# Kernel optimization log

Measured on AMD Instinct MI355X. Metric: run time of the kernel, lower is better.

The kernel has to match this reference:

```python
import jax, jax.numpy as jnp
import numpy as np

NUM_GROUPS = 32
EPS = 1e-6


def group_norm(x, scale, bias):
    # x: [b, c, l]
    b, c, l = x.shape
    xg = x.reshape(b, NUM_GROUPS, (c // NUM_GROUPS) * l)
    mean = jnp.mean(xg, axis=2, keepdims=True)
    var = jnp.var(xg, axis=2, keepdims=True)
    xn = ((xg - mean) * jax.lax.rsqrt(var + EPS)).reshape(b, c, l)
    return xn * scale[None, :, None] + bias[None, :, None]


def conv1x1(x, w, b):
    # pointwise conv: w [out_c, in_c], x [b, in_c, l]
    return jnp.einsum('oc,bcl->bol', w, x) + b[None, :, None]


def setup_inputs() -> dict:
    key = jax.random.key(0)
    ks = jax.random.split(key, 11)
    b, c, l = 4, 512, 4096
    s = 1.0 / np.sqrt(c)
    return {
        'x': jax.random.normal(ks[0], (b, c, l), jnp.float32),
        'gn_scale': jnp.ones((c,), jnp.float32),
        'gn_bias': jnp.zeros((c,), jnp.float32),
        'wq': jax.random.normal(ks[1], (c, c), jnp.float32) * s,
        'bq': jnp.zeros((c,), jnp.float32),
        'wk': jax.random.normal(ks[2], (c, c), jnp.float32) * s,
        'bk': jnp.zeros((c,), jnp.float32),
        'wv': jax.random.normal(ks[3], (c, c), jnp.float32) * s,
        'bv': jnp.zeros((c,), jnp.float32),
        'wp': jax.random.normal(ks[4], (c, c), jnp.float32) * s,
        'bp': jnp.zeros((c,), jnp.float32),
    }


def reference(x, gn_scale, gn_bias, wq, bq, wk, bk, wv, bv, wp, bp):
    h_ = group_norm(x, gn_scale, gn_bias)
    q = conv1x1(h_, wq, bq)  # [b, c, l]
    k = conv1x1(h_, wk, bk)
    v = conv1x1(h_, wv, bv)
    c = q.shape[1]
    # scores w[b,i,j] = sum_c q[b,c,i] k[b,c,j] * c^-0.5, softmax over j
    w = jnp.einsum('bci,bcj->bij', q, k) * (c ** -0.5)
    w = jax.nn.softmax(w, axis=2)
    # out[b,c,i] = sum_j w[b,i,j] v[b,c,j]
    h_ = jnp.einsum('bij,bcj->bci', w, v)
    h_ = conv1x1(h_, wp, bp)
    return x + h_
```

## Files before the change

kernel.cpp:

```cpp
#include <hip/hip_runtime.h>
#include <math.h>

#define BB 4
#define CC 512
#define LL 4096
#define NG 32
#define CPG 16
#define EPSV 1e-6f

typedef short s16x8 __attribute__((ext_vector_type(8)));
typedef __bf16 bf8v __attribute__((ext_vector_type(8)));
typedef float f32x4 __attribute__((ext_vector_type(4)));
typedef unsigned short u16;
typedef unsigned char u8;

typedef const __attribute__((address_space(1))) void g1_void;
typedef __attribute__((address_space(3))) void l3_void;

#define ASM_SBAR() asm volatile("s_barrier" ::: "memory")
#define ASM_WAITV(N) asm volatile("s_waitcnt vmcnt(" #N ")" ::: "memory")

static __device__ __forceinline__ float bf2f(u16 h) {
    unsigned int u = ((unsigned int)h) << 16;
    union { unsigned int u; float f; } c; c.u = u; return c.f;
}
static __device__ __forceinline__ u16 f2bf(float f) {
    union { float f; unsigned int u; } c; c.f = f;
    unsigned int lsb = (c.u >> 16) & 1u;
    c.u += 0x7fffu + lsb;
    return (u16)(c.u >> 16);
}
static __device__ __forceinline__ u8 f2fp8(float f) {
    int v = __builtin_amdgcn_cvt_pk_fp8_f32(f, f, 0, false);
    return (u8)(v & 0xff);
}
static __device__ __forceinline__ bf8v ld_bf8(const u16* p) {
    return *reinterpret_cast<const bf8v*>(p);
}
static __device__ __forceinline__ void gload16(const u16* g, u16* l) {
    __builtin_amdgcn_global_load_lds((g1_void*)g, (l3_void*)l, 16, 0, 0);
}
static __device__ __forceinline__ void gload16b(const u8* g, u8* l) {
    __builtin_amdgcn_global_load_lds((g1_void*)g, (l3_void*)l, 16, 0, 0);
}

__global__ __launch_bounds__(256) void zero_kernel(float* __restrict__ p, int n) {
    int i = blockIdx.x * 256 + threadIdx.x;
    if (i < n) p[i] = 0.f;
}

__global__ __launch_bounds__(256) void wconv_kernel(const float* __restrict__ w0,
                                                    const float* __restrict__ w1,
                                                    const float* __restrict__ w2,
                                                    const float* __restrict__ w3,
                                                    u16* __restrict__ wbf) {
    int i = blockIdx.x * 256 + threadIdx.x;
    int wsel = blockIdx.y;
    const float* src = (wsel == 0) ? w0 : (wsel == 1) ? w1 : (wsel == 2) ? w2 : w3;
    float4 v = reinterpret_cast<const float4*>(src)[i];
    ushort4 o;
    o.x = f2bf(v.x); o.y = f2bf(v.y); o.z = f2bf(v.z); o.w = f2bf(v.w);
    reinterpret_cast<ushort4*>(wbf + (size_t)wsel * CC * CC)[i] = o;
}

__global__ __launch_bounds__(256) void biascat_kernel(const float* __restrict__ bq,
                                                      const float* __restrict__ bk,
                                                      const float* __restrict__ bv,
                                                      float* __restrict__ bcat) {
    int i = blockIdx.x * 256 + threadIdx.x;
    if (i >= 3 * CC) return;
    float v = (i < CC) ? bq[i] : (i < 2 * CC ? bk[i - CC] : bv[i - 2 * CC]);
    bcat[i] = v;
}

__global__ __launch_bounds__(256) void gn_stats_kernel(const float* __restrict__ x,
                                                       float2* __restrict__ stats) {
    int g = blockIdx.x, b = blockIdx.y, t = threadIdx.x;
    const float4* xp = reinterpret_cast<const float4*>(x + ((size_t)b * CC + (size_t)g * CPG) * LL);
    float s = 0.f, ss = 0.f;
    for (int it = 0; it < 64; ++it) {
        float4 v = xp[it * 256 + t];
        s += v.x + v.y + v.z + v.w;
        ss += v.x * v.x + v.y * v.y + v.z * v.z + v.w * v.w;
    }
    #pragma unroll
    for (int off = 32; off; off >>= 1) { s += __shfl_xor(s, off, 64); ss += __shfl_xor(ss, off, 64); }
    __shared__ float rs[4], rss[4];
    int wave = t >> 6, lane = t & 63;
    if (lane == 0) { rs[wave] = s; rss[wave] = ss; }
    __syncthreads();
    if (t == 0) {
        float S = rs[0] + rs[1] + rs[2] + rs[3];
        float SS = rss[0] + rss[1] + rss[2] + rss[3];
        float mean = S * (1.f / 65536.f);
        float var = SS * (1.f / 65536.f) - mean * mean;
        var = fmaxf(var, 0.f);
        stats[b * NG + g] = make_float2(mean, rsqrtf(var + EPSV));
    }
}

__global__ __launch_bounds__(256) void gn_norm_t_kernel(const float* __restrict__ x,
                                                        const float2* __restrict__ stats,
                                                        const float* __restrict__ gsc,
                                                        const float* __restrict__ gbi,
                                                        u16* __restrict__ hT) {
    int lt = blockIdx.x, ct = blockIdx.y, b = blockIdx.z;
    __shared__ u16 tile[64][72];
    int t = threadIdx.x;
    int cl0 = t >> 4, c4 = (t & 15) * 4;
    #pragma unroll
    for (int p = 0; p < 4; ++p) {
        int cl = p * 16 + cl0;
        int cg = ct * 64 + cl;
        float2 st = stats[b * NG + (cg >> 4)];
        float sc = gsc[cg] * st.y;
        float bi = gbi[cg];
        float4 v = *reinterpret_cast<const float4*>(x + ((size_t)b * CC + cg) * LL + lt * 64 + c4);
        tile[cl][c4 + 0] = f2bf((v.x - st.x) * sc + bi);
        tile[cl][c4 + 1] = f2bf((v.y - st.x) * sc + bi);
        tile[cl][c4 + 2] = f2bf((v.z - st.x) * sc + bi);
        tile[cl][c4 + 3] = f2bf((v.w - st.x) * sc + bi);
    }
    __syncthreads();
    int r = t >> 3, c8 = (t & 7) * 8;
    #pragma unroll
    for (int p = 0; p < 2; ++p) {
        int ll = p * 32 + r;
        s16x8 ov;
        #pragma unroll
        for (int j = 0; j < 8; ++j) ov[j] = (short)tile[c8 + j][ll];
        u16* hp = hT + ((size_t)b * LL + lt * 64 + ll) * CC + ct * 64 + c8;
        *reinterpret_cast<s16x8*>(hp) = ov;
    }
}

template <int MODE>
__global__ __launch_bounds__(256) void gemm_kernel(const u16* __restrict__ A, size_t asb, int lda,
                                                   const u16* __restrict__ B, size_t bsb, int ldb,
                                                   const float* __restrict__ bias,
                                                   u8* __restrict__ Oq, u8* __restrict__ Ok,
                                                   u8* __restrict__ Ov, size_t osb,
                                                   const float* __restrict__ xres,
                                                   float* __restrict__ fout, int K) {
    __shared__ u16 pool[17408];
    u8* pool8 = (u8*)pool;
    int mt = blockIdx.x, nt = blockIdx.y, b = blockIdx.z;
    int t = threadIdx.x;
    int wave = t >> 6, lane = t & 63;
    int wm = (wave >> 1) * 64, wn = (wave & 1) * 64;
    int l15 = lane & 15, quad = lane >> 4;
    f32x4 acc[4][4] = {};
    const u16* Ab = A + (size_t)b * asb + (size_t)mt * 128 * lda;
    const u16* Bb = B + (size_t)b * bsb + (size_t)nt * 128 * ldb;
    int swzg = ((lane & 3) ^ ((lane >> 2) & 3) ^ ((lane >> 4) & 3)) * 8;
    int row0 = wave * 16 + (lane >> 2);
    int row1 = 64 + row0;
    const u16* Ap0 = Ab + (size_t)row0 * lda + swzg;
    const u16* Ap1 = Ab + (size_t)row1 * lda + swzg;
    const u16* Bp0 = Bb + (size_t)row0 * ldb + swzg;
    const u16* Bp1 = Bb + (size_t)row1 * ldb + swzg;
    int wo = wave * 512;
    int swzf = (l15 & 3) ^ (l15 >> 2);
    int aoff = (wm + l15) * 32 + ((quad ^ swzf) * 8);
    int boff = (wn + l15) * 32 + ((quad ^ swzf) * 8);
    const int iters = K >> 5;
    gload16(Ap0, pool + wo);                gload16(Ap1, pool + 2048 + wo);
    gload16(Bp0, pool + 8192 + wo);         gload16(Bp1, pool + 8192 + 2048 + wo);
    gload16(Ap0 + 32, pool + 4096 + wo);    gload16(Ap1 + 32, pool + 4096 + 2048 + wo);
    gload16(Bp0 + 32, pool + 12288 + wo);   gload16(Bp1 + 32, pool + 12288 + 2048 + wo);
    for (int i = 0; i < iters; ++i) {
        if (i + 1 < iters) { ASM_WAITV(4); } else { ASM_WAITV(0); }
        ASM_SBAR();
        int bs = (i & 1) * 4096;
        const u16* As = pool + bs;
        const u16* Bs = pool + 8192 + bs;
        bf8v af[4], bfr[4];
        #pragma unroll
        for (int ii = 0; ii < 4; ++ii)
            af[ii] = ld_bf8(&As[aoff + ii * 512]);
        #pragma unroll
        for (int j = 0; j < 4; ++j)
            bfr[j] = ld_bf8(&Bs[boff + j * 512]);
        #pragma unroll
        for (int ii = 0; ii < 4; ++ii)
            #pragma unroll
            for (int j = 0; j < 4; ++j)
                acc[ii][j] = __builtin_amdgcn_mfma_f32_16x16x32_bf16(af[ii], bfr[j], acc[ii][j], 0, 0, 0);
        ASM_SBAR();
        if (i + 2 < iters) {
            int kk = (i + 2) * 32;
            u16* as = pool + bs; u16* bsp = pool + 8192 + bs;
            gload16(Ap0 + kk, as + wo);        gload16(Ap1 + kk, as + 2048 + wo);
            gload16(Bp0 + kk, bsp + wo);       gload16(Bp1 + kk, bsp + 2048 + wo);
        }
    }
    __syncthreads();
    if (MODE == 0) {
        int nt_sel = nt >> 2, ntl = nt & 3;
        bool transT = (nt_sel == 2);
        #pragma unroll
        for (int j = 0; j < 4; ++j) {
            float bv = bias[nt * 128 + wn + j * 16 + l15];
            #pragma unroll
            for (int i = 0; i < 4; ++i) {
                if (transT) {
                    int col = wn + j * 16 + l15;
                    int row = wm + i * 16 + quad * 4;
                    unsigned int w = __builtin_amdgcn_cvt_pk_fp8_f32(acc[i][j][0] + bv, acc[i][j][1] + bv, 0, false);
                    w = __builtin_amdgcn_cvt_pk_fp8_f32(acc[i][j][2] + bv, acc[i][j][3] + bv, w, true);
                    *reinterpret_cast<unsigned int*>(&pool8[col * 144 + row]) = w;
                } else {
                    #pragma unroll
                    for (int r = 0; r < 4; ++r) {
                        int row = wm + i * 16 + quad * 4 + r;
                        int col = wn + j * 16 + l15;
                        pool8[row * 144 + col] = f2fp8(acc[i][j][r] + bv);
                    }
                }
            }
        }
        __syncthreads();
        u8* Ob; int rstride;
        if (nt_sel == 0)      { Ob = Oq + (size_t)b * osb + (size_t)(mt * 128) * CC + ntl * 128; rstride = CC; }
        else if (nt_sel == 1) { Ob = Ok + (size_t)b * osb + (size_t)(mt * 128) * CC + ntl * 128; rstride = CC; }
        else                  { Ob = Ov + (size_t)b * osb + (size_t)(ntl * 128) * LL + mt * 128; rstride = LL; }
        #pragma unroll
        for (int it = 0; it < 4; ++it) {
            int idx = it * 256 + t;
            int row = idx >> 3, ch = (idx & 7) * 16;
            *reinterpret_cast<float4*>(Ob + (size_t)row * rstride + ch) =
                *reinterpret_cast<const float4*>(&pool8[row * 144 + ch]);
        }
    } else {
        #pragma unroll
        for (int j = 0; j < 4; ++j) {
            float bv = bias[nt * 128 + wn + j * 16 + l15];
            #pragma unroll
            for (int i = 0; i < 4; ++i)
                #pragma unroll
                for (int r = 0; r < 4; ++r) {
                    int row = wm + i * 16 + quad * 4 + r;
                    int col = wn + j * 16 + l15;
                    pool[col * 136 + row] = f2bf(acc[i][j][r] + bv);
                }
        }
        __syncthreads();
        const float* xb = xres + ((size_t)b * CC + nt * 128) * LL + mt * 128;
        float* ob = fout + ((size_t)b * CC + nt * 128) * LL + mt * 128;
        #pragma unroll
        for (int it = 0; it < 16; ++it) {
            int idx = it * 256 + t;
            int cl = idx >> 5, ch = (idx & 31) * 4;
            short4 pv = *reinterpret_cast<const short4*>(&pool[cl * 136 + ch]);
            float4 xv = *reinterpret_cast<const float4*>(xb + (size_t)cl * LL + ch);
            float4 ov;
            ov.x = xv.x + bf2f((u16)pv.x);
            ov.y = xv.y + bf2f((u16)pv.y);
            ov.z = xv.z + bf2f((u16)pv.z);
            ov.w = xv.w + bf2f((u16)pv.w);
            *reinterpret_cast<float4*>(ob + (size_t)cl * LL + ch) = ov;
        }
    }
}

template <int MODE>
__global__ __launch_bounds__(256) void gemm8_kernel(const u8* __restrict__ A, size_t asb, int lda,
                                                    const u8* __restrict__ B, size_t bsb, int ldb,
                                                    float scale,
                                                    u8* __restrict__ Out8, u16* __restrict__ OutH,
                                                    size_t osb, int Nout, int K,
                                                    float* __restrict__ rsum) {
    __shared__ u8 pool8[MODE == 1 ? 18432 : 34816];
    int mt = blockIdx.x, nt = blockIdx.y, b = blockIdx.z;
    int t = threadIdx.x;
    int wave = t >> 6, lane = t & 63;
    int wm = (wave >> 1) * 64, wn = (wave & 1) * 64;
    int l15 = lane & 15, quad = lane >> 4;
    f32x4 acc[4][4] = {};
    int R = wave * 32 + (lane >> 1);
    int c16 = ((lane & 1) ^ (R & 1) ^ ((R >> 2) & 1)) * 16;
    const u8* Ap = A + (size_t)b * asb + (size_t)(mt * 128 + R) * lda + c16;
    const u8* Bp = B + (size_t)b * bsb + (size_t)(nt * 128 + R) * ldb + c16;
    u8* ldsw = pool8 + wave * 1024;
    int p = (l15 & 1) ^ ((l15 >> 2) & 1);
    int fo = (((quad >> 1) ^ p) * 16) + (quad & 1) * 8;
    int abase = (wm + l15) * 32 + fo;
    int bbase = (wn + l15) * 32 + fo;
    const int iters = K >> 5;
    gload16b(Ap, ldsw);                 gload16b(Bp, pool8 + 8192 + wave * 1024);
    gload16b(Ap + 32, pool8 + 4096 + wave * 1024);
    gload16b(Bp + 32, pool8 + 12288 + wave * 1024);
    for (int i = 0; i < iters; ++i) {
        if (i + 1 < iters) { ASM_WAITV(2); } else { ASM_WAITV(0); }
        ASM_SBAR();
        int bs = (i & 1) * 4096;
        const u8* As = pool8 + bs;
        const u8* Bs = pool8 + 8192 + bs;
        long af[4], bfr[4];
        #pragma unroll
        for (int ii = 0; ii < 4; ++ii)
            af[ii] = *reinterpret_cast<const long*>(As + abase + ii * 512);
        #pragma unroll
        for (int j = 0; j < 4; ++j)
            bfr[j] = *reinterpret_cast<const long*>(Bs + bbase + j * 512);
        #pragma unroll
        for (int ii = 0; ii < 4; ++ii)
            #pragma unroll
            for (int j = 0; j < 4; ++j)
                acc[ii][j] = __builtin_amdgcn_mfma_f32_16x16x32_fp8_fp8(af[ii], bfr[j], acc[ii][j], 0, 0, 0);
        ASM_SBAR();
        if (i + 2 < iters) {
            int kk = (i + 2) * 32;
            gload16b(Ap + kk, pool8 + bs + wave * 1024);
            gload16b(Bp + kk, pool8 + 8192 + bs + wave * 1024);
        }
    }
    __syncthreads();
    if (MODE == 1) {
        #pragma unroll
        for (int i = 0; i < 4; ++i) {
            #pragma unroll
            for (int r = 0; r < 4; ++r) {
                int row = wm + i * 16 + quad * 4 + r;
                float part = 0.f;
                #pragma unroll
                for (int j = 0; j < 4; ++j) {
                    float v = __expf(acc[i][j][r] * scale - 3.0f);
                    part += v;
                    pool8[row * 144 + wn + j * 16 + l15] = f2fp8(v);
                }
                part += __shfl_xor(part, 1, 64);
                part += __shfl_xor(part, 2, 64);
                part += __shfl_xor(part, 4, 64);
                part += __shfl_xor(part, 8, 64);
                if (l15 == 0)
                    atomicAdd(rsum + (size_t)b * LL + mt * 128 + row, part);
            }
        }
        __syncthreads();
        u8* Ob = Out8 + (size_t)b * osb + (size_t)(mt * 128) * Nout + nt * 128;
        #pragma unroll
        for (int it = 0; it < 4; ++it) {
            int idx = it * 256 + t;
            int row = idx >> 3, ch = (idx & 7) * 16;
            *reinterpret_cast<float4*>(Ob + (size_t)row * Nout + ch) =
                *reinterpret_cast<const float4*>(&pool8[row * 144 + ch]);
        }
    } else {
        u16* poolh = (u16*)pool8;
        float invl[4][4];
        #pragma unroll
        for (int i = 0; i < 4; ++i)
            #pragma unroll
            for (int r = 0; r < 4; ++r)
                invl[i][r] = 1.f / rsum[(size_t)b * LL + mt * 128 + wm + i * 16 + quad * 4 + r];
        #pragma unroll
        for (int j = 0; j < 4; ++j)
            #pragma unroll
            for (int i = 0; i < 4; ++i)
                #pragma unroll
                for (int r = 0; r < 4; ++r) {
                    int row = wm + i * 16 + quad * 4 + r;
                    int col = wn + j * 16 + l15;
                    poolh[row * 136 + col] = f2bf(acc[i][j][r] * invl[i][r]);
                }
        __syncthreads();
        u16* Ob = OutH + (size_t)b * osb + (size_t)(mt * 128) * Nout + nt * 128;
        #pragma unroll
        for (int it = 0; it < 8; ++it) {
            int idx = it * 256 + t;
            int row = idx >> 4, ch = (idx & 15) * 8;
            s16x8 val = *reinterpret_cast<const s16x8*>(&poolh[row * 136 + ch]);
            *reinterpret_cast<s16x8*>(Ob + (size_t)row * Nout + ch) = val;
        }
    }
}

extern "C" void kernel_launch(void* const* d_in, const int* in_sizes, int n_in,
                              void* d_out, int out_size, void* d_ws, size_t ws_size,
                              hipStream_t stream) {
    const float* x   = (const float*)d_in[0];
    const float* gsc = (const float*)d_in[1];
    const float* gbi = (const float*)d_in[2];
    const float* wq  = (const float*)d_in[3];
    const float* bq  = (const float*)d_in[4];
    const float* wk  = (const float*)d_in[5];
    const float* bk  = (const float*)d_in[6];
    const float* wv  = (const float*)d_in[7];
    const float* bv  = (const float*)d_in[8];
    const float* wp  = (const float*)d_in[9];
    const float* bp  = (const float*)d_in[10];
    float* out = (float*)d_out;

    char* ws = (char*)d_ws;
    const size_t SZ   = (size_t)BB * LL * CC * 2;
    const size_t QSZ  = (size_t)BB * LL * CC;
    const size_t WQSZ = (size_t)4 * CC * CC * 2;
    const size_t RSZ  = (size_t)BB * LL * 4;
    u16* bufA = (u16*)(ws);
    u8*  q8   = (u8*)(ws + SZ);
    u8*  k8   = (u8*)(ws + SZ + QSZ);
    u8*  v8   = (u8*)(ws + SZ + 2 * QSZ);
    u16* wbf  = (u16*)(ws + SZ + 3 * QSZ);
    float2* stats = (float2*)(ws + SZ + 3 * QSZ + WQSZ);
    float* bcat   = (float*)(ws + SZ + 3 * QSZ + WQSZ + 4096);
    float* rowsum = (float*)(ws + SZ + 3 * QSZ + WQSZ + 4096 + 8192);
    u8* S8 = (u8*)(ws + SZ + 3 * QSZ + WQSZ + 4096 + 8192 + RSZ);
    const float scale = 0.044194173824159216f;
    const size_t BLC = (size_t)LL * CC;

    wconv_kernel<<<dim3(256, 4), 256, 0, stream>>>(wq, wk, wv, wp, wbf);
    biascat_kernel<<<dim3(6), 256, 0, stream>>>(bq, bk, bv, bcat);
    gn_stats_kernel<<<dim3(NG, BB), 256, 0, stream>>>(x, stats);
    gn_norm_t_kernel<<<dim3(64, 8, BB), 256, 0, stream>>>(x, stats, gsc, gbi, bufA);
    gemm_kernel<0><<<dim3(32, 12, BB), 256, 0, stream>>>(bufA, BLC, CC, wbf, 0, CC, bcat,
                                                         q8, k8, v8, BLC, nullptr, nullptr, CC);
    zero_kernel<<<dim3((BB * LL + 255) / 256), 256, 0, stream>>>(rowsum, BB * LL);
    gemm8_kernel<1><<<dim3(32, 32, BB), 256, 0, stream>>>(q8, BLC, CC, k8, BLC, CC, scale,
                                                          S8, nullptr, (size_t)LL * LL, LL, CC, rowsum);
    gemm8_kernel<2><<<dim3(32, 4, BB), 256, 0, stream>>>(S8, (size_t)LL * LL, LL, v8, BLC, LL, 1.f,
                                                         nullptr, bufA, BLC, CC, LL, rowsum);
    gemm_kernel<3><<<dim3(32, 4, BB), 256, 0, stream>>>(bufA, BLC, CC, wbf + 3 * CC * CC, 0, CC,
                                                        bp, nullptr, nullptr, nullptr, 0, x, out, CC);
}
```

Before: 322.7 us.

## Deepen fp8 GEMM K-stage, write epilogues directly to global, fuse rowsum zeroing

Measured after the change: 310.9 us. 1.04x faster.

```diff
diff --git a/kernel.cpp b/kernel.cpp
--- a/kernel.cpp
+++ b/kernel.cpp
@@ -42,11 +42,6 @@
 }
 static __device__ __forceinline__ void gload16b(const u8* g, u8* l) {
     __builtin_amdgcn_global_load_lds((g1_void*)g, (l3_void*)l, 16, 0, 0);
-}
-
-__global__ __launch_bounds__(256) void zero_kernel(float* __restrict__ p, int n) {
-    int i = blockIdx.x * 256 + threadIdx.x;
-    if (i < n) p[i] = 0.f;
 }
 
 __global__ __launch_bounds__(256) void wconv_kernel(const float* __restrict__ w0,
@@ -66,11 +61,14 @@
 __global__ __launch_bounds__(256) void biascat_kernel(const float* __restrict__ bq,
                                                       const float* __restrict__ bk,
                                                       const float* __restrict__ bv,
-                                                      float* __restrict__ bcat) {
+                                                      float* __restrict__ bcat,
+                                                      float* __restrict__ rowsum) {
     int i = blockIdx.x * 256 + threadIdx.x;
-    if (i >= 3 * CC) return;
-    float v = (i < CC) ? bq[i] : (i < 2 * CC ? bk[i - CC] : bv[i - 2 * CC]);
-    bcat[i] = v;
+    if (i < 3 * CC) {
+        float v = (i < CC) ? bq[i] : (i < 2 * CC ? bk[i - CC] : bv[i - 2 * CC]);
+        bcat[i] = v;
+    }
+    if (i < BB * LL) rowsum[i] = 0.f;
 }
 
 __global__ __launch_bounds__(256) void gn_stats_kernel(const float* __restrict__ x,
@@ -194,44 +192,48 @@
             gload16(Bp0 + kk, bsp + wo);       gload16(Bp1 + kk, bsp + 2048 + wo);
         }
     }
-    __syncthreads();
     if (MODE == 0) {
         int nt_sel = nt >> 2, ntl = nt & 3;
-        bool transT = (nt_sel == 2);
-        #pragma unroll
-        for (int j = 0; j < 4; ++j) {
-            float bv = bias[nt * 128 + wn + j * 16 + l15];
-            #pragma unroll
-            for (int i = 0; i < 4; ++i) {
-                if (transT) {
+        if (nt_sel == 2) {
+            __syncthreads();
+            #pragma unroll
+            for (int j = 0; j < 4; ++j) {
+                float bv = bias[nt * 128 + wn + j * 16 + l15];
+                #pragma unroll
+                for (int i = 0; i < 4; ++i) {
                     int col = wn + j * 16 + l15;
                     int row = wm + i * 16 + quad * 4;
                     unsigned int w = __builtin_amdgcn_cvt_pk_fp8_f32(acc[i][j][0] + bv, acc[i][j][1] + bv, 0, false);
                     w = __builtin_amdgcn_cvt_pk_fp8_f32(acc[i][j][2] + bv, acc[i][j][3] + bv, w, true);
                     *reinterpret_cast<unsigned int*>(&pool8[col * 144 + row]) = w;
-                } else {
+                }
+            }
+            __syncthreads();
+            u8* Ob = Ov + (size_t)b * osb + (size_t)(ntl * 128) * LL + mt * 128;
+            #pragma unroll
+            for (int it = 0; it < 4; ++it) {
+                int idx = it * 256 + t;
+                int row = idx >> 3, ch = (idx & 7) * 16;
+                *reinterpret_cast<float4*>(Ob + (size_t)row * LL + ch) =
+                    *reinterpret_cast<const float4*>(&pool8[row * 144 + ch]);
+            }
+        } else {
+            u8* Oc = (nt_sel == 0 ? Oq : Ok) + (size_t)b * osb
+                     + (size_t)(mt * 128) * CC + ntl * 128 + wn + l15;
+            #pragma unroll
+            for (int j = 0; j < 4; ++j) {
+                float bv = bias[nt * 128 + wn + j * 16 + l15];
+                #pragma unroll
+                for (int i = 0; i < 4; ++i)
                     #pragma unroll
                     for (int r = 0; r < 4; ++r) {
                         int row = wm + i * 16 + quad * 4 + r;
-                        int col = wn + j * 16 + l15;
-                        pool8[row * 144 + col] = f2fp8(acc[i][j][r] + bv);
+                        Oc[(size_t)row * CC + j * 16] = f2fp8(acc[i][j][r] + bv);
                     }
-                }
             }
         }
+    } else {
         __syncthreads();
-        u8* Ob; int rstride;
-        if (nt_sel == 0)      { Ob = Oq + (size_t)b * osb + (size_t)(mt * 128) * CC + ntl * 128; rstride = CC; }
-        else if (nt_sel == 1) { Ob = Ok + (size_t)b * osb + (size_t)(mt * 128) * CC + ntl * 128; rstride = CC; }
-        else                  { Ob = Ov + (size_t)b * osb + (size_t)(ntl * 128) * LL + mt * 128; rstride = LL; }
-        #pragma unroll
-        for (int it = 0; it < 4; ++it) {
-            int idx = it * 256 + t;
-            int row = idx >> 3, ch = (idx & 7) * 16;
-            *reinterpret_cast<float4*>(Ob + (size_t)row * rstride + ch) =
-                *reinterpret_cast<const float4*>(&pool8[row * 144 + ch]);
-        }
-    } else {
         #pragma unroll
         for (int j = 0; j < 4; ++j) {
             float bv = bias[nt * 128 + wn + j * 16 + l15];
@@ -270,7 +272,7 @@
                                                     u8* __restrict__ Out8, u16* __restrict__ OutH,
                                                     size_t osb, int Nout, int K,
                                                     float* __restrict__ rsum) {
-    __shared__ u8 pool8[MODE == 1 ? 18432 : 34816];
+    __shared__ u8 pool8[MODE == 1 ? 32768 : 34816];
     int mt = blockIdx.x, nt = blockIdx.y, b = blockIdx.z;
     int t = threadIdx.x;
     int wave = t >> 6, lane = t & 63;
@@ -281,53 +283,58 @@
     int c16 = ((lane & 1) ^ (R & 1) ^ ((R >> 2) & 1)) * 16;
     const u8* Ap = A + (size_t)b * asb + (size_t)(mt * 128 + R) * lda + c16;
     const u8* Bp = B + (size_t)b * bsb + (size_t)(nt * 128 + R) * ldb + c16;
-    u8* ldsw = pool8 + wave * 1024;
+    int wo = wave * 1024;
     int p = (l15 & 1) ^ ((l15 >> 2) & 1);
     int fo = (((quad >> 1) ^ p) * 16) + (quad & 1) * 8;
     int abase = (wm + l15) * 32 + fo;
     int bbase = (wn + l15) * 32 + fo;
-    const int iters = K >> 5;
-    gload16b(Ap, ldsw);                 gload16b(Bp, pool8 + 8192 + wave * 1024);
-    gload16b(Ap + 32, pool8 + 4096 + wave * 1024);
-    gload16b(Bp + 32, pool8 + 12288 + wave * 1024);
+    const int iters = K >> 6;
+    #define STG(ii, bsv) do { int kk = (ii) * 64;                          \
+        gload16b(Ap + kk,      pool8 + (bsv) + wo);                        \
+        gload16b(Ap + kk + 32, pool8 + (bsv) + 4096 + wo);                 \
+        gload16b(Bp + kk,      pool8 + 16384 + (bsv) + wo);                \
+        gload16b(Bp + kk + 32, pool8 + 16384 + (bsv) + 4096 + wo); } while (0)
+    STG(0, 0);
+    STG(1, 8192);
     for (int i = 0; i < iters; ++i) {
-        if (i + 1 < iters) { ASM_WAITV(2); } else { ASM_WAITV(0); }
+        if (i + 1 < iters) { ASM_WAITV(4); } else { ASM_WAITV(0); }
         ASM_SBAR();
-        int bs = (i & 1) * 4096;
+        int bs = (i & 1) * 8192;
         const u8* As = pool8 + bs;
-        const u8* Bs = pool8 + 8192 + bs;
-        long af[4], bfr[4];
-        #pragma unroll
-        for (int ii = 0; ii < 4; ++ii)
-            af[ii] = *reinterpret_cast<const long*>(As + abase + ii * 512);
-        #pragma unroll
-        for (int j = 0; j < 4; ++j)
-            bfr[j] = *reinterpret_cast<const long*>(Bs + bbase + j * 512);
-        #pragma unroll
-        for (int ii = 0; ii < 4; ++ii)
+        const u8* Bs = pool8 + 16384 + bs;
+        #pragma unroll
+        for (int h = 0; h < 2; ++h) {
+            long af[4], bfr[4];
+            #pragma unroll
+            for (int ii = 0; ii < 4; ++ii)
+                af[ii] = *reinterpret_cast<const long*>(As + h * 4096 + abase + ii * 512);
             #pragma unroll
             for (int j = 0; j < 4; ++j)
-                acc[ii][j] = __builtin_amdgcn_mfma_f32_16x16x32_fp8_fp8(af[ii], bfr[j], acc[ii][j], 0, 0, 0);
+                bfr[j] = *reinterpret_cast<const long*>(Bs + h * 4096 + bbase + j * 512);
+            #pragma unroll
+            for (int ii = 0; ii < 4; ++ii)
+                #pragma unroll
+                for (int j = 0; j < 4; ++j)
+                    acc[ii][j] = __builtin_amdgcn_mfma_f32_16x16x32_fp8_fp8(af[ii], bfr[j], acc[ii][j], 0, 0, 0);
+        }
         ASM_SBAR();
-        if (i + 2 < iters) {
-            int kk = (i + 2) * 32;
-            gload16b(Ap + kk, pool8 + bs + wave * 1024);
-            gload16b(Bp + kk, pool8 + 8192 + bs + wave * 1024);
-        }
-    }
-    __syncthreads();
+        if (i + 2 < iters) STG(i + 2, bs);
+    }
+    #undef STG
     if (MODE == 1) {
+        u8* Ob = Out8 + (size_t)b * osb + (size_t)(mt * 128) * Nout + nt * 128 + wn + l15;
         #pragma unroll
         for (int i = 0; i < 4; ++i) {
             #pragma unroll
             for (int r = 0; r < 4; ++r) {
                 int row = wm + i * 16 + quad * 4 + r;
+                u8* rp = Ob + (size_t)row * Nout;
                 float part = 0.f;
                 #pragma unroll
                 for (int j = 0; j < 4; ++j) {
                     float v = __expf(acc[i][j][r] * scale - 3.0f);
                     part += v;
-                    pool8[row * 144 + wn + j * 16 + l15] = f2fp8(v);
+                    rp[j * 16] = f2fp8(v);
                 }
                 part += __shfl_xor(part, 1, 64);
                 part += __shfl_xor(part, 2, 64);
@@ -337,16 +344,8 @@
                     atomicAdd(rsum + (size_t)b * LL + mt * 128 + row, part);
             }
         }
+    } else {
         __syncthreads();
-        u8* Ob = Out8 + (size_t)b * osb + (size_t)(mt * 128) * Nout + nt * 128;
-        #pragma unroll
-        for (int it = 0; it < 4; ++it) {
-            int idx = it * 256 + t;
-            int row = idx >> 3, ch = (idx & 7) * 16;
-            *reinterpret_cast<float4*>(Ob + (size_t)row * Nout + ch) =
-                *reinterpret_cast<const float4*>(&pool8[row * 144 + ch]);
-        }
-    } else {
         u16* poolh = (u16*)pool8;
         float invl[4][4];
         #pragma unroll
@@ -410,12 +409,11 @@
     const size_t BLC = (size_t)LL * CC;
 
     wconv_kernel<<<dim3(256, 4), 256, 0, stream>>>(wq, wk, wv, wp, wbf);
-    biascat_kernel<<<dim3(6), 256, 0, stream>>>(bq, bk, bv, bcat);
+    biascat_kernel<<<dim3(64), 256, 0, stream>>>(bq, bk, bv, bcat, rowsum);
     gn_stats_kernel<<<dim3(NG, BB), 256, 0, stream>>>(x, stats);
     gn_norm_t_kernel<<<dim3(64, 8, BB), 256, 0, stream>>>(x, stats, gsc, gbi, bufA);
     gemm_kernel<0><<<dim3(32, 12, BB), 256, 0, stream>>>(bufA, BLC, CC, wbf, 0, CC, bcat,
                                                          q8, k8, v8, BLC, nullptr, nullptr, CC);
-    zero_kernel<<<dim3((BB * LL + 255) / 256), 256, 0, stream>>>(rowsum, BB * LL);
     gemm8_kernel<1><<<dim3(32, 32, BB), 256, 0, stream>>>(q8, BLC, CC, k8, BLC, CC, scale,
                                                           S8, nullptr, (size_t)LL * LL, LL, CC, rowsum);
     gemm8_kernel<2><<<dim3(32, 4, BB), 256, 0, stream>>>(S8, (size_t)LL * LL, LL, v8, BLC, LL, 1.f,
```
